# Performance work log

Hardware: AMD Instinct MI355X
Metric: run time of the kernel (lower is better)

## Reference

```python
import jax, jax.numpy as jnp
import numpy as np

B, T, D, H, DK, DV, C, M = 8, 512, 1024, 8, 128, 128, 512, 512
TAU = float(DK) ** 0.5

def _ln(x, g, b, eps=1e-6):
    mu = x.mean(-1, keepdims=True)
    var = ((x - mu) ** 2).mean(-1, keepdims=True)
    return (x - mu) * jax.lax.rsqrt(var + eps) * g + b

def _hln(x, eps=1e-6):
    mu = x.mean(-1, keepdims=True)
    var = ((x - mu) ** 2).mean(-1, keepdims=True)
    return (x - mu) * jax.lax.rsqrt(var + eps)

def setup_inputs() -> dict:
    key = jax.random.key(0)
    ks = jax.random.split(key, 14)
    s = lambda k, shape, fan: jax.random.normal(k, shape, jnp.float32) * (fan ** -0.5)
    return {
        "x": jax.random.normal(ks[0], (B, T, D), jnp.float32),
        "doc_ids": jax.random.randint(ks[1], (B, T), 0, 4),
        "loss_mask": jnp.ones((B, T), jnp.float32),
        "xl_k_hat": jax.random.normal(ks[2], (B, H, M, DK), jnp.float32),
        "xl_v": jax.random.normal(ks[3], (B, H, M, DV), jnp.float32),
        "agg_upper": jax.random.normal(ks[4], (B, H, C, DV), jnp.float32),
        "agg_lower": jax.random.uniform(ks[5], (B, H, C), jnp.float32) * 8.0,
        "w_ln_g": jnp.ones((D,), jnp.float32),
        "w_ln_b": jnp.zeros((D,), jnp.float32),
        "w_q": s(ks[6], (D, H * DK), D),
        "w_k": s(ks[7], (D, H * DK), D),
        "w_v": s(ks[8], (D, H * DV), D),
        "w_g": s(ks[9], (D, H * DV), D),
        "w_res": s(ks[10], (H * DV, D), H * DV),
        "x_u": jax.random.normal(ks[11], (H, DK), jnp.float32) * 0.02,
        "codebook": jax.random.normal(ks[12], (H, C, DK), jnp.float32),
    }

def reference(x, doc_ids, loss_mask, xl_k_hat, xl_v, agg_upper, agg_lower,
              w_ln_g, w_ln_b, w_q, w_k, w_v, w_g, w_res, x_u, codebook):
    # ---- compute_k_q_v_g ----
    xt = _ln(x, w_ln_g, w_ln_b)                                  # [B,T,D]
    q = _hln((xt @ w_q).reshape(B, T, H, DK).transpose(0, 2, 1, 3))  # [B,H,T,DK]
    k = _hln((xt @ w_k).reshape(B, T, H, DK).transpose(0, 2, 1, 3))  # [B,H,T,DK]
    v = (xt @ w_v).reshape(B, T, H, DV).transpose(0, 2, 1, 3)        # [B,H,T,DV]
    g = jax.nn.silu(xt @ w_g)                                        # [B,T,H*DV]

    # ---- vector quantize keys (LearnableVQ) ----
    # dist[b,h,t,c] = ||k - codebook||^2 ; argmin -> shortcodes z
    kc = jnp.einsum('bhtd,hcd->bhtc', k, codebook)
    dist = (k ** 2).sum(-1)[..., None] - 2.0 * kc + (codebook ** 2).sum(-1)[None, :, None, :]
    z = jnp.argmin(dist, axis=-1)                                 # [B,H,T] shortcodes
    k_hat = codebook[jnp.arange(H)[None, :, None], z]             # [B,H,T,DK]
    k_hat_st = k + jax.lax.stop_gradient(k_hat - k)               # straight-through
    mask = loss_mask[:, None, :]                                  # [B,1,T]
    denom_m = mask.sum() * H + 1e-6
    l_commit = (((k - jax.lax.stop_gradient(k_hat)) ** 2).sum(-1) * mask).sum() / denom_m
    l_codebook = (((jax.lax.stop_gradient(k) - k_hat) ** 2).sum(-1) * mask).sum() / denom_m

    # ---- attention over xlcache ++ present, plus aggregated codeword cache ----
    recent_k = jnp.concatenate([xl_k_hat, k_hat_st], axis=2)      # [B,H,M+T,DK]
    recent_v = jnp.concatenate([xl_v, v], axis=2)                 # [B,H,M+T,DV]
    qb = q + x_u[None, :, None, :]
    s_rec = jnp.einsum('bhtd,bhsd->bhts', qb, recent_k) / TAU     # [B,H,T,M+T]
    s_agg = jnp.einsum('bhtd,hcd->bhtc', qb, codebook) / TAU      # [B,H,T,C]

    i = jnp.arange(T)[:, None]
    j = jnp.arange(M + T)[None, :]
    allow = ((j - M) <= i).astype(s_rec.dtype)                    # causal over recent window
    NEG = jnp.asarray(-1e30, s_rec.dtype)
    s_rec_m = jnp.where(allow > 0, s_rec, NEG)

    m = jnp.maximum(s_rec_m.max(-1), s_agg.max(-1))               # [B,H,T]
    a_rec = jnp.exp(s_rec_m - m[..., None]) * allow               # [B,H,T,M+T]
    a_agg = jnp.exp(s_agg - m[..., None])                         # [B,H,T,C]
    den = a_rec.sum(-1) + jnp.einsum('bhtc,bhc->bht', a_agg, agg_lower)
    num = (jnp.einsum('bhts,bhsd->bhtd', a_rec, recent_v)
           + jnp.einsum('bhtc,bhcd->bhtd', a_agg, agg_upper))
    wv = num / den[..., None]                                     # [B,H,T,DV]

    o = wv.transpose(0, 2, 1, 3).reshape(B, T, H * DV) * g        # gated
    res = o @ w_res                                               # [B,T,D]
    return res, l_commit, l_codebook
```

## Files before the change

kernel.cpp:

```cpp
#include <hip/hip_runtime.h>
#include <math.h>

namespace {

constexpr int nB = 8, nT = 512, nD = 1024, nH = 8, nDK = 128, nDV = 128, nC = 512, nM = 512;
constexpr int NROW = nB * nT;
constexpr float RTAU = 0.08838834764831845f;

typedef __attribute__((ext_vector_type(8))) short short8;
typedef __attribute__((ext_vector_type(4))) float f32x4;

__device__ __forceinline__ ushort f2bf(float f) {
  union { float f; uint u; } x; x.f = f;
  uint r = x.u + 0x7fff + ((x.u >> 16) & 1);
  return (ushort)(r >> 16);
}
__device__ __forceinline__ uint pk2(float a, float b) {
  return (uint)f2bf(a) | ((uint)f2bf(b) << 16);
}
__device__ __forceinline__ float bf2f(ushort u) {
  return __uint_as_float(((uint)u) << 16);
}
__device__ __forceinline__ void gload16(const void* g, void* l) {
  __builtin_amdgcn_global_load_lds((const __attribute__((address_space(1))) void*)g,
                                   (__attribute__((address_space(3))) void*)l, 16, 0, 0);
}

constexpr int PREP_LN = 4096;
constexpr int PREP_CAST = PREP_LN + 12288;
constexpr int PREP_WT = PREP_CAST + 1280;
constexpr int PREP_CB = PREP_WT + 2048;

__global__ __launch_bounds__(256) void prep_kernel(
    const float* __restrict__ x, const float* __restrict__ gw, const float* __restrict__ bw,
    ushort* __restrict__ xt_bf,
    const float* __restrict__ xlk, ushort* __restrict__ xlk_bf,
    const float* __restrict__ xlv, ushort* __restrict__ xlv_bf,
    const float* __restrict__ aggU, ushort* __restrict__ aggU_bf,
    const float* __restrict__ wq, const float* __restrict__ wk, const float* __restrict__ wv,
    const float* __restrict__ wg, const float* __restrict__ wres,
    ushort* __restrict__ wqkvg_t, ushort* __restrict__ wres_t,
    const float* __restrict__ cb, float* __restrict__ cbn, ushort* __restrict__ cb_bf) {
  __shared__ float tile[64][65];
  __shared__ float smc[4];
  const int bid = blockIdx.x;
  const int tid = threadIdx.x;

  if (bid < PREP_LN) {
    size_t row = bid;
    float4 v = ((const float4*)(x + row * nD))[tid];
    {
      int lane = tid & 63, w = tid >> 6;
      float s = v.x + v.y + v.z + v.w;
#pragma unroll
      for (int off = 32; off; off >>= 1) s += __shfl_down(s, off);
      if (lane == 0) smc[w] = s;
    }
    __syncthreads();
    float mu = (smc[0] + smc[1] + smc[2] + smc[3]) * (1.f / nD);
    __syncthreads();
    float4 d = make_float4(v.x - mu, v.y - mu, v.z - mu, v.w - mu);
    {
      int lane = tid & 63, w = tid >> 6;
      float s = d.x * d.x + d.y * d.y + d.z * d.z + d.w * d.w;
#pragma unroll
      for (int off = 32; off; off >>= 1) s += __shfl_down(s, off);
      if (lane == 0) smc[w] = s;
    }
    __syncthreads();
    float var = (smc[0] + smc[1] + smc[2] + smc[3]) * (1.f / nD);
    float rs = rsqrtf(var + 1e-6f);
    float4 gg = ((const float4*)gw)[tid];
    float4 bb = ((const float4*)bw)[tid];
    uint2 pb;
    pb.x = pk2(d.x * rs * gg.x + bb.x, d.y * rs * gg.y + bb.y);
    pb.y = pk2(d.z * rs * gg.z + bb.z, d.w * rs * gg.w + bb.w);
    ((uint2*)(xt_bf + row * nD))[tid] = pb;
  } else if (bid < PREP_CAST) {
    const int i = bid - PREP_LN;
    const int which = i >> 12, blk = i & 4095;
    const float* src = which == 0 ? xlk : (which == 1 ? xlv : aggU);
    ushort* dst = which == 0 ? xlk_bf : (which == 1 ? xlv_bf : aggU_bf);
    size_t idx = (size_t)blk * 256 + tid;
    float4 v = ((const float4*)src)[idx];
    uint2 p;
    p.x = pk2(v.x, v.y);
    p.y = pk2(v.z, v.w);
    ((uint2*)dst)[idx] = p;
  } else if (bid < PREP_WT) {
    const int i = bid - PREP_CAST;
    const int z = i >> 8, rem = i & 255;
    const int kz = (rem >> 4) * 64, nz = (rem & 15) * 64;
    const float* W;
    ushort* D;
    if (z == 0)      { W = wq;   D = wqkvg_t; }
    else if (z == 1) { W = wk;   D = wqkvg_t + (size_t)1024 * 1024; }
    else if (z == 2) { W = wv;   D = wqkvg_t + (size_t)2048 * 1024; }
    else if (z == 3) { W = wg;   D = wqkvg_t + (size_t)3072 * 1024; }
    else             { W = wres; D = wres_t; }
    const int c = tid & 63, r4 = tid >> 6;
#pragma unroll
    for (int k = 0; k < 16; ++k) {
      int r = k * 4 + r4;
      tile[r][c] = W[(size_t)(kz + r) * 1024 + nz + c];
    }
    __syncthreads();
#pragma unroll
    for (int k = 0; k < 16; ++k) {
      int n = k * 4 + r4;
      D[(size_t)(nz + n) * 1024 + kz + c] = f2bf(tile[c][n]);
    }
  } else {
    const int i = bid - PREP_WT;
    const int grp = tid >> 7, t128 = tid & 127;
    const int hc = i * 2 + grp;
    float v = cb[(size_t)hc * 128 + t128];
    cb_bf[(size_t)hc * 128 + t128] = f2bf(v);
    float s = v * v;
#pragma unroll
    for (int off = 32; off; off >>= 1) s += __shfl_down(s, off);
    if ((t128 & 63) == 0) smc[grp * 2 + (t128 >> 6)] = s;
    __syncthreads();
    if (t128 == 0) cbn[hc] = smc[grp * 2] + smc[grp * 2 + 1];
  }
}

template <int MODE>
__global__ __launch_bounds__(256) void gemm_bf16_kernel(const ushort* __restrict__ A,
                                                        const ushort* __restrict__ Bt,
                                                        float* __restrict__ C0,
                                                        ushort* __restrict__ C1,
                                                        ushort* __restrict__ C2,
                                                        ushort* __restrict__ C3,
                                                        ushort* __restrict__ kbf,
                                                        float* __restrict__ knorm2,
                                                        const float* __restrict__ xu) {
  __shared__ __align__(16) ushort As[128 * 32];
  __shared__ __align__(16) ushort Bs[128 * 32];
  __shared__ float rowsum[128][2];
  __shared__ float rowsum2[128][2];
  const int tid = threadIdx.x;
  const int w = tid >> 6, l = tid & 63;
  const int lr = l & 15, lg = l >> 4;
  const int wr = w >> 1, wc = w & 1;
  const int n0 = blockIdx.x * 128;
  const int m0 = blockIdx.y * 128;
  constexpr int K = 1024;

  f32x4 acc[4][4];
#pragma unroll
  for (int i = 0; i < 4; ++i)
#pragma unroll
    for (int j = 0; j < 4; ++j) acc[i][j] = (f32x4){0.f, 0.f, 0.f, 0.f};

  const int e0 = w * 512 + l * 8;
  const int r0 = e0 >> 5, c0 = e0 & 31;
  const int e1 = 2048 + e0;
  const int r1 = e1 >> 5, c1 = e1 & 31;
  const ushort* a0p = A + (size_t)(m0 + r0) * K + c0;
  const ushort* a1p = A + (size_t)(m0 + r1) * K + c1;
  const ushort* b0p = Bt + (size_t)(n0 + r0) * K + c0;
  const ushort* b1p = Bt + (size_t)(n0 + r1) * K + c1;
  ushort* lA0 = &As[w * 512];
  ushort* lA1 = &As[2048 + w * 512];
  ushort* lB0 = &Bs[w * 512];
  ushort* lB1 = &Bs[2048 + w * 512];

  for (int k0 = 0; k0 < K; k0 += 32) {
    __syncthreads();
    gload16(a0p + k0, lA0);
    gload16(a1p + k0, lA1);
    gload16(b0p + k0, lB0);
    gload16(b1p + k0, lB1);
    __syncthreads();
    short8 af[4], bfr[4];
#pragma unroll
    for (int i = 0; i < 4; ++i) af[i] = *(const short8*)&As[(wr * 64 + i * 16 + lr) * 32 + lg * 8];
#pragma unroll
    for (int j = 0; j < 4; ++j) bfr[j] = *(const short8*)&Bs[(wc * 64 + j * 16 + lr) * 32 + lg * 8];
    __builtin_amdgcn_s_setprio(1);
#pragma unroll
    for (int i = 0; i < 4; ++i)
#pragma unroll
      for (int j = 0; j < 4; ++j)
        acc[i][j] = __builtin_amdgcn_mfma_f32_16x16x32_bf16(af[i], bfr[j], acc[i][j], 0, 0, 0);
    __builtin_amdgcn_s_setprio(0);
  }

  const int seg = n0 >> 10;
  const int nbase = n0 & 1023;
  if (MODE == 1 && seg <= 1) {
    const int h = nbase >> 7;
    float ps[4][4], ps2[4][4];
#pragma unroll
    for (int i = 0; i < 4; ++i)
#pragma unroll
      for (int r2 = 0; r2 < 4; ++r2) {
        float s = 0.f, s2 = 0.f;
#pragma unroll
        for (int j = 0; j < 4; ++j) {
          float v = acc[i][j][r2];
          s += v;
          s2 += v * v;
        }
#pragma unroll
        for (int off = 1; off < 16; off <<= 1) {
          s += __shfl_xor(s, off);
          s2 += __shfl_xor(s2, off);
        }
        ps[i][r2] = s;
        ps2[i][r2] = s2;
      }
    if (lr == 0) {
#pragma unroll
      for (int i = 0; i < 4; ++i)
#pragma unroll
        for (int r2 = 0; r2 < 4; ++r2) {
          int rloc = wr * 64 + i * 16 + lg * 4 + r2;
          rowsum[rloc][wc] = ps[i][r2];
          rowsum2[rloc][wc] = ps2[i][r2];
        }
    }
    __syncthreads();
#pragma unroll
    for (int i = 0; i < 4; ++i)
#pragma unroll
      for (int r2 = 0; r2 < 4; ++r2) {
        const int rloc = wr * 64 + i * 16 + lg * 4 + r2;
        const int grow = m0 + rloc;
        float tot = rowsum[rloc][0] + rowsum[rloc][1];
        float tot2 = rowsum2[rloc][0] + rowsum2[rloc][1];
        float mu = tot * (1.f / 128.f);
        float qf = tot2 - 128.f * mu * mu;
        float rs = rsqrtf(qf * (1.f / 128.f) + 1e-6f);
#pragma unroll
        for (int j = 0; j < 4; ++j) {
          const int col = wc * 64 + j * 16 + lr;
          float v = (acc[i][j][r2] - mu) * rs;
          if (seg == 0) {
            v += xu[h * 128 + col];
            C1[(size_t)grow * 1024 + nbase + col] = f2bf(v);
          } else {
            kbf[(size_t)grow * 1024 + nbase + col] = f2bf(v);
          }
        }
        if (seg == 1 && lr == 0 && wc == 0) knorm2[(size_t)grow * 8 + h] = qf * rs * rs;
      }
  } else {
#pragma unroll
    for (int i = 0; i < 4; ++i)
#pragma unroll
      for (int j = 0; j < 4; ++j)
#pragma unroll
        for (int r2 = 0; r2 < 4; ++r2) {
          const int row = m0 + wr * 64 + i * 16 + lg * 4 + r2;
          const int col = wc * 64 + j * 16 + lr;
          float v = acc[i][j][r2];
          if (MODE == 0) {
            C0[(size_t)row * 1024 + n0 + col] = v;
          } else {
            const int nloc = nbase + col;
            if (seg == 2) {
              C2[(size_t)row * 1024 + nloc] = f2bf(v);
            } else {
              float s = v / (1.f + __expf(-v));
              C3[(size_t)row * 1024 + nloc] = f2bf(s);
            }
          }
        }
  }
}

__global__ __launch_bounds__(256) void vq_mfma_kernel(const ushort* __restrict__ kbf,
                                                      const ushort* __restrict__ cb_bf,
                                                      const float* __restrict__ cbn,
                                                      const float* __restrict__ knorm2,
                                                      const float* __restrict__ mask,
                                                      ushort* __restrict__ khat_bf,
                                                      float* __restrict__ blocksq) {
  __shared__ ushort Kb[64][136];
  __shared__ ushort Cb[64][136];
  __shared__ float cnsh[64];
  __shared__ int zsh[64];
  __shared__ float dsh[64];
  const int tid = threadIdx.x;
  const int w = tid >> 6, l = tid & 63;
  const int lr = l & 15, lg = l >> 4;
  const int b = blockIdx.y >> 3, h = blockIdx.y & 7;
  const int t0 = blockIdx.x * 64;
  const int srow = tid >> 2, sd = (tid & 3) * 32;

  {
    const ushort* src = kbf + ((size_t)((b * nT + t0 + srow) * nH + h)) * 128 + sd;
    *(uint4*)&Kb[srow][sd] = *(const uint4*)src;
    *(uint4*)&Kb[srow][sd + 8] = *(const uint4*)(src + 8);
    *(uint4*)&Kb[srow][sd + 16] = *(const uint4*)(src + 16);
    *(uint4*)&Kb[srow][sd + 24] = *(const uint4*)(src + 24);
  }
  __syncthreads();

  short8 af[4];
#pragma unroll
  for (int k0 = 0; k0 < 4; ++k0) af[k0] = *(const short8*)&Kb[w * 16 + lr][k0 * 32 + lg * 8];

  float best[4] = {1e30f, 1e30f, 1e30f, 1e30f};
  int bidx[4] = {0, 0, 0, 0};

  for (int cc = 0; cc < 8; ++cc) {
    __syncthreads();
    {
      const ushort* src = cb_bf + ((size_t)(h * nC + cc * 64 + srow)) * 128 + sd;
      *(uint4*)&Cb[srow][sd] = *(const uint4*)src;
      *(uint4*)&Cb[srow][sd + 8] = *(const uint4*)(src + 8);
      *(uint4*)&Cb[srow][sd + 16] = *(const uint4*)(src + 16);
      *(uint4*)&Cb[srow][sd + 24] = *(const uint4*)(src + 24);
      if (tid < 64) cnsh[tid] = cbn[h * nC + cc * 64 + tid];
    }
    __syncthreads();
#pragma unroll
    for (int ct = 0; ct < 4; ++ct) {
      f32x4 z = (f32x4){0.f, 0.f, 0.f, 0.f};
#pragma unroll
      for (int k0 = 0; k0 < 4; ++k0) {
        short8 cf = *(const short8*)&Cb[ct * 16 + lr][k0 * 32 + lg * 8];
        z = __builtin_amdgcn_mfma_f32_16x16x32_bf16(af[k0], cf, z, 0, 0, 0);
      }
      const int code = cc * 64 + ct * 16 + lr;
      const float cn = cnsh[ct * 16 + lr];
#pragma unroll
      for (int r2 = 0; r2 < 4; ++r2) {
        float d = cn - 2.f * z[r2];
        if (d < best[r2]) { best[r2] = d; bidx[r2] = code; }
      }
    }
  }

#pragma unroll
  for (int off = 1; off < 16; off <<= 1) {
#pragma unroll
    for (int r2 = 0; r2 < 4; ++r2) {
      float od = __shfl_xor(best[r2], off);
      int oi = __shfl_xor(bidx[r2], off);
      if (od < best[r2] || (od == best[r2] && oi < bidx[r2])) { best[r2] = od; bidx[r2] = oi; }
    }
  }
  if (lr == 0) {
#pragma unroll
    for (int r2 = 0; r2 < 4; ++r2) {
      int row = w * 16 + lg * 4 + r2;
      zsh[row] = bidx[r2];
      dsh[row] = best[r2];
    }
  }
  __syncthreads();

  {
    const int row = tid >> 2, part = (tid & 3) * 32;
    const ushort* src = cb_bf + ((size_t)(h * nC + zsh[row])) * 128 + part;
    ushort* dst = khat_bf + ((size_t)((b * nT + t0 + row) * nH + h)) * 128 + part;
    *(uint4*)dst = *(const uint4*)src;
    *(uint4*)(dst + 8) = *(const uint4*)(src + 8);
    *(uint4*)(dst + 16) = *(const uint4*)(src + 16);
    *(uint4*)(dst + 24) = *(const uint4*)(src + 24);
  }

  if (tid < 64) {
    float s = mask[b * nT + t0 + tid] *
              (knorm2[(size_t)(b * nT + t0 + tid) * nH + h] + dsh[tid]);
#pragma unroll
    for (int off = 32; off; off >>= 1) s += __shfl_down(s, off);
    if (tid == 0) blocksq[blockIdx.y * gridDim.x + blockIdx.x] = s;
  }
}

__global__ __launch_bounds__(256) void attn_mfma_kernel(
    const ushort* __restrict__ qb, const ushort* __restrict__ khat,
    const ushort* __restrict__ vbuf, const ushort* __restrict__ xlk,
    const ushort* __restrict__ xlv, const ushort* __restrict__ cbb,
    const ushort* __restrict__ aggU, const float* __restrict__ aggL,
    const ushort* __restrict__ gbuf, ushort* __restrict__ o) {
  __shared__ ushort Ks[64][136];
  __shared__ ushort Vts[128][72];
  __shared__ ushort Ps[4][16][72];
  __shared__ float lowb[64];

  const int tid = threadIdx.x;
  const int w = tid >> 6, l = tid & 63;
  const int lr = l & 15, lg = l >> 4;
  const int b = blockIdx.x >> 3, h = blockIdx.x & 7;
  const int t0 = blockIdx.y * 64;

  short8 qf[4];
  {
    const ushort* qrow = qb + ((size_t)((b * nT + t0 + w * 16 + lr) * nH + h)) * 128;
#pragma unroll
    for (int k0 = 0; k0 < 4; ++k0) qf[k0] = *(const short8*)(qrow + k0 * 32 + lg * 8);
  }

  float m_r[4] = {-1e30f, -1e30f, -1e30f, -1e30f};
  float l_r[4] = {0.f, 0.f, 0.f, 0.f};
  f32x4 acc_o[8];
#pragma unroll
  for (int dt = 0; dt < 8; ++dt) acc_o[dt] = (f32x4){0.f, 0.f, 0.f, 0.f};

  const int srow = tid >> 2, sd = (tid & 3) * 32;
  const int kp = tid & 31, dbase = (tid >> 5) * 16;

  auto stageK = [&](const ushort* src) {
#pragma unroll
    for (int q4 = 0; q4 < 4; ++q4)
      *(uint4*)&Ks[srow][sd + q4 * 8] = *(const uint4*)(src + q4 * 8);
  };
  auto stageVbf = [&](const ushort* v0, const ushort* v1) {
    short8 a0 = *(const short8*)(v0);
    short8 a1 = *(const short8*)(v0 + 8);
    short8 b0 = *(const short8*)(v1);
    short8 b1 = *(const short8*)(v1 + 8);
#pragma unroll
    for (int i2 = 0; i2 < 8; ++i2) {
      *(uint*)&Vts[dbase + i2][2 * kp] = (uint)(ushort)a0[i2] | ((uint)(ushort)b0[i2] << 16);
      *(uint*)&Vts[dbase + 8 + i2][2 * kp] = (uint)(ushort)a1[i2] | ((uint)(ushort)b1[i2] << 16);
    }
  };

  auto chunk_body = [&](int sbase, bool AGG, bool MASKQ) {
    f32x4 sc[4];
    __builtin_amdgcn_s_setprio(1);
#pragma unroll
    for (int kt = 0; kt < 4; ++kt) {
      f32x4 z = (f32x4){0.f, 0.f, 0.f, 0.f};
#pragma unroll
      for (int k0 = 0; k0 < 4; ++k0) {
        short8 kf = *(const short8*)&Ks[kt * 16 + lr][k0 * 32 + lg * 8];
        z = __builtin_amdgcn_mfma_f32_16x16x32_bf16(qf[k0], kf, z, 0, 0, 0);
      }
      sc[kt] = z;
    }
    __builtin_amdgcn_s_setprio(0);
    float sv[4][4];
    float pm[4] = {-1e30f, -1e30f, -1e30f, -1e30f};
#pragma unroll
    for (int kt = 0; kt < 4; ++kt)
#pragma unroll
      for (int r2 = 0; r2 < 4; ++r2) {
        float s = sc[kt][r2] * RTAU;
        if (MASKQ) {
          int key = sbase + kt * 16 + lr;
          int tl = t0 + w * 16 + lg * 4 + r2 + nM;
          if (key > tl) s = -1e30f;
        }
        sv[kt][r2] = s;
        pm[r2] = fmaxf(pm[r2], s);
      }
#pragma unroll
    for (int r2 = 0; r2 < 4; ++r2)
#pragma unroll
      for (int off = 1; off < 16; off <<= 1) pm[r2] = fmaxf(pm[r2], __shfl_xor(pm[r2], off));
    float scale[4], rs[4];
#pragma unroll
    for (int r2 = 0; r2 < 4; ++r2) {
      float mn = fmaxf(m_r[r2], pm[r2]);
      scale[r2] = __expf(m_r[r2] - mn);
      m_r[r2] = mn;
      rs[r2] = 0.f;
    }
#pragma unroll
    for (int kt = 0; kt < 4; ++kt)
#pragma unroll
      for (int r2 = 0; r2 < 4; ++r2) {
        float p = __expf(sv[kt][r2] - m_r[r2]);
        rs[r2] += AGG ? p * lowb[kt * 16 + lr] : p;
        Ps[w][lg * 4 + r2][kt * 16 + lr] = f2bf(p);
      }
#pragma unroll
    for (int r2 = 0; r2 < 4; ++r2)
#pragma unroll
      for (int off = 1; off < 16; off <<= 1) rs[r2] += __shfl_xor(rs[r2], off);
#pragma unroll
    for (int r2 = 0; r2 < 4; ++r2) l_r[r2] = l_r[r2] * scale[r2] + rs[r2];
#pragma unroll
    for (int dt = 0; dt < 8; ++dt)
#pragma unroll
      for (int r2 = 0; r2 < 4; ++r2) acc_o[dt][r2] *= scale[r2];
    short8 pa0 = *(const short8*)&Ps[w][lr][lg * 8];
    short8 pa1 = *(const short8*)&Ps[w][lr][32 + lg * 8];
    __builtin_amdgcn_s_setprio(1);
#pragma unroll
    for (int dt = 0; dt < 8; ++dt) {
      short8 vf0 = *(const short8*)&Vts[dt * 16 + lr][lg * 8];
      short8 vf1 = *(const short8*)&Vts[dt * 16 + lr][32 + lg * 8];
      acc_o[dt] = __builtin_amdgcn_mfma_f32_16x16x32_bf16(pa0, vf0, acc_o[dt], 0, 0, 0);
      acc_o[dt] = __builtin_amdgcn_mfma_f32_16x16x32_bf16(pa1, vf1, acc_o[dt], 0, 0, 0);
    }
    __builtin_amdgcn_s_setprio(0);
  };

  const int nch = t0 / 64 + 9;
  for (int ci = 0; ci < nch; ++ci) {
    const int sbase = ci * 64;
    __syncthreads();
    {
      int s = sbase + srow;
      const ushort* src = (s < nM)
          ? xlk + ((size_t)(b * nH + h) * nM + s) * 128 + sd
          : khat + ((size_t)((b * nT + (s - nM)) * nH + h)) * 128 + sd;
      stageK(src);
    }
    {
      int s0 = sbase + 2 * kp;
      if (s0 < nM) {
        const ushort* v0 = xlv + ((size_t)(b * nH + h) * nM + s0) * 128 + dbase;
        stageVbf(v0, v0 + 128);
      } else {
        const ushort* v0 = vbuf + ((size_t)((b * nT + (s0 - nM)) * nH + h)) * 128 + dbase;
        stageVbf(v0, v0 + nH * 128);
      }
    }
    __syncthreads();
    chunk_body(sbase, false, ci == nch - 1);
  }

  for (int ca = 0; ca < 8; ++ca) {
    const int sbase = ca * 64;
    __syncthreads();
    stageK(cbb + ((size_t)h * nC + sbase + srow) * 128 + sd);
    {
      const ushort* v0 = aggU + ((size_t)(b * nH + h) * nC + sbase + 2 * kp) * 128 + dbase;
      stageVbf(v0, v0 + 128);
    }
    if (tid < 64) lowb[tid] = aggL[(size_t)(b * nH + h) * nC + sbase + tid];
    __syncthreads();
    chunk_body(sbase, true, false);
  }

  float inv[4];
#pragma unroll
  for (int r2 = 0; r2 < 4; ++r2) inv[r2] = 1.f / l_r[r2];
#pragma unroll
  for (int dt = 0; dt < 8; ++dt)
#pragma unroll
    for (int r2 = 0; r2 < 4; ++r2) {
      int trow = t0 + w * 16 + lg * 4 + r2;
      size_t oi = ((size_t)(b * nT + trow)) * nD + h * 128 + dt * 16 + lr;
      float gv = bf2f(gbuf[oi]);
      o[oi] = f2bf(acc_o[dt][r2] * inv[r2] * gv);
    }
}

__global__ __launch_bounds__(256) void finalize_kernel(const float* __restrict__ blocksq,
                                                       int nblk,
                                                       const float* __restrict__ mask,
                                                       float* __restrict__ outp) {
  __shared__ float sm[8];
  const int tid = threadIdx.x;
  float s = 0.f, ms = 0.f;
  for (int i = tid; i < NROW; i += 256) {
    if (i < nblk) s += blocksq[i];
    ms += mask[i];
  }
#pragma unroll
  for (int off = 32; off; off >>= 1) { s += __shfl_down(s, off); ms += __shfl_down(ms, off); }
  if ((tid & 63) == 0) { sm[tid >> 6] = s; sm[4 + (tid >> 6)] = ms; }
  __syncthreads();
  if (tid == 0) {
    float ts = sm[0] + sm[1] + sm[2] + sm[3];
    float tm = sm[4] + sm[5] + sm[6] + sm[7];
    float l = ts / (tm * (float)nH + 1e-6f);
    outp[0] = l;
    outp[1] = l;
  }
}

}

extern "C" void kernel_launch(void* const* d_in, const int* in_sizes, int n_in,
                              void* d_out, int out_size, void* d_ws, size_t ws_size,
                              hipStream_t stream) {
  const float* x    = (const float*)d_in[0];
  const float* mask = (const float*)d_in[2];
  const float* xlk  = (const float*)d_in[3];
  const float* xlv  = (const float*)d_in[4];
  const float* aggU = (const float*)d_in[5];
  const float* aggL = (const float*)d_in[6];
  const float* wlng = (const float*)d_in[7];
  const float* wlnb = (const float*)d_in[8];
  const float* wq   = (const float*)d_in[9];
  const float* wk   = (const float*)d_in[10];
  const float* wv   = (const float*)d_in[11];
  const float* wg   = (const float*)d_in[12];
  const float* wres = (const float*)d_in[13];
  const float* xu   = (const float*)d_in[14];
  const float* cb   = (const float*)d_in[15];
  float* out = (float*)d_out;

  float* ws = (float*)d_ws;
  const size_t SZ = (size_t)NROW * nD;
  float*  kregion = ws;
  ushort* qbuf_bf = (ushort*)(ws + SZ);
  ushort* khat_bf = (ushort*)(ws + SZ + SZ / 2);
  ushort* vbuf_bf = (ushort*)(ws + 2 * SZ);
  ushort* gbuf_bf = (ushort*)(ws + 2 * SZ + SZ / 2);
  ushort* xt_bf   = (ushort*)(ws + 3 * SZ);
  ushort* wqkvg_t = (ushort*)(ws + 3 * SZ + SZ / 2);
  ushort* wres_t  = (ushort*)(ws + 4 * SZ);
  ushort* xlk_bf  = (ushort*)(ws + 4 * SZ + SZ / 8);
  ushort* xlv_bf  = (ushort*)(ws + 4 * SZ + SZ / 8 + SZ / 2);
  ushort* aggU_bf = (ushort*)(ws + 4 * SZ + SZ / 8 + SZ);
  ushort* cb_bf   = (ushort*)(ws + 4 * SZ + SZ / 8 + 3 * SZ / 2);
  float*  cbn     = ws + 4 * SZ + SZ / 8 + 3 * SZ / 2 + SZ / 16;
  float*  knorm2  = cbn + 4096;
  float*  bsq     = knorm2 + 32768;
  ushort* kbf     = (ushort*)kregion;
  ushort* obuf_bf = xt_bf;

  prep_kernel<<<PREP_CB, 256, 0, stream>>>(
      x, wlng, wlnb, xt_bf, xlk, xlk_bf, xlv, xlv_bf, aggU, aggU_bf,
      wq, wk, wv, wg, wres, wqkvg_t, wres_t, cb, cbn, cb_bf);

  gemm_bf16_kernel<1><<<dim3(32, 32), 256, 0, stream>>>(
      xt_bf, wqkvg_t, nullptr, qbuf_bf, vbuf_bf, gbuf_bf, kbf, knorm2, xu);

  vq_mfma_kernel<<<dim3(nT / 64, nB * nH), 256, 0, stream>>>(kbf, cb_bf, cbn, knorm2,
                                                             mask, khat_bf, bsq);

  attn_mfma_kernel<<<dim3(nB * nH, nT / 64), 256, 0, stream>>>(
      qbuf_bf, khat_bf, vbuf_bf, xlk_bf, xlv_bf, cb_bf, aggU_bf, aggL, gbuf_bf, obuf_bf);

  gemm_bf16_kernel<0><<<dim3(8, 32), 256, 0, stream>>>(
      obuf_bf, wres_t, out, nullptr, nullptr, nullptr, nullptr, nullptr, nullptr);
  finalize_kernel<<<1, 256, 0, stream>>>(bsq, nT / 64 * nB * nH, mask, out + SZ);
}
```

Measured before the change: 231.2 us.

## Pre-transpose V operands and double-buffer attention staging with async LDS loads

V-like operands (xl_v, agg_upper, and the projected V) are now stored transposed in bf16: the prep kernel does it for xl_v and agg_upper, and the QKV GEMM epilogue does it for V through an LDS tile. The attention kernel then stages K and V^T tiles with direct global-to-LDS loads into XOR-swizzled, double-buffered shared memory, prefetching the next chunk while computing the current one, and uses one barrier per chunk. This removes the per-chunk register-level V transpose and the two-barrier stage-then-compute serialization. In exchange it adds a transposing epilogue with extra syncs in the GEMM, more shared memory (possibly lowering occupancy), and swizzle indexing that must match between writer and reader.

```diff
diff --git a/kernel.cpp b/kernel.cpp
--- a/kernel.cpp
+++ b/kernel.cpp
@@ -25,18 +25,24 @@
   __builtin_amdgcn_global_load_lds((const __attribute__((address_space(1))) void*)g,
                                    (__attribute__((address_space(3))) void*)l, 16, 0, 0);
 }
+__device__ __forceinline__ void gload4(const void* g, void* l) {
+  __builtin_amdgcn_global_load_lds((const __attribute__((address_space(1))) void*)g,
+                                   (__attribute__((address_space(3))) void*)l, 4, 0, 0);
+}
 
 constexpr int PREP_LN = 4096;
-constexpr int PREP_CAST = PREP_LN + 12288;
-constexpr int PREP_WT = PREP_CAST + 1280;
-constexpr int PREP_CB = PREP_WT + 2048;
+constexpr int PREP_XLK = PREP_LN + 4096;
+constexpr int PREP_XLVT = PREP_XLK + 1024;
+constexpr int PREP_AGGUT = PREP_XLVT + 1024;
+constexpr int PREP_WT = PREP_AGGUT + 1280;
+constexpr int PREP_TOTAL = PREP_WT + 2048;
 
 __global__ __launch_bounds__(256) void prep_kernel(
     const float* __restrict__ x, const float* __restrict__ gw, const float* __restrict__ bw,
     ushort* __restrict__ xt_bf,
     const float* __restrict__ xlk, ushort* __restrict__ xlk_bf,
-    const float* __restrict__ xlv, ushort* __restrict__ xlv_bf,
-    const float* __restrict__ aggU, ushort* __restrict__ aggU_bf,
+    const float* __restrict__ xlv, ushort* __restrict__ xlvT,
+    const float* __restrict__ aggU, ushort* __restrict__ aggUT,
     const float* __restrict__ wq, const float* __restrict__ wk, const float* __restrict__ wv,
     const float* __restrict__ wg, const float* __restrict__ wres,
     ushort* __restrict__ wqkvg_t, ushort* __restrict__ wres_t,
@@ -76,19 +82,37 @@
     pb.x = pk2(d.x * rs * gg.x + bb.x, d.y * rs * gg.y + bb.y);
     pb.y = pk2(d.z * rs * gg.z + bb.z, d.w * rs * gg.w + bb.w);
     ((uint2*)(xt_bf + row * nD))[tid] = pb;
-  } else if (bid < PREP_CAST) {
-    const int i = bid - PREP_LN;
-    const int which = i >> 12, blk = i & 4095;
-    const float* src = which == 0 ? xlk : (which == 1 ? xlv : aggU);
-    ushort* dst = which == 0 ? xlk_bf : (which == 1 ? xlv_bf : aggU_bf);
+  } else if (bid < PREP_XLK) {
+    const int blk = bid - PREP_LN;
     size_t idx = (size_t)blk * 256 + tid;
-    float4 v = ((const float4*)src)[idx];
+    float4 v = ((const float4*)xlk)[idx];
     uint2 p;
     p.x = pk2(v.x, v.y);
     p.y = pk2(v.z, v.w);
-    ((uint2*)dst)[idx] = p;
+    ((uint2*)xlk_bf)[idx] = p;
+  } else if (bid < PREP_AGGUT) {
+    const bool isXlv = bid < PREP_XLVT;
+    const int i = bid - (isXlv ? PREP_XLK : PREP_XLVT);
+    const float* S = isXlv ? xlv : aggU;
+    ushort* D = isXlv ? xlvT : aggUT;
+    const int bh = i >> 4, t = i & 15;
+    const int tok0 = (t >> 1) * 64, d0 = (t & 1) * 64;
+    const float* src = S + ((size_t)bh * 512 + tok0) * 128 + d0;
+    ushort* dst = D + ((size_t)bh * 128 + d0) * 512 + tok0;
+    const int c = tid & 63, r4 = tid >> 6;
+#pragma unroll
+    for (int k = 0; k < 16; ++k) {
+      int r = k * 4 + r4;
+      tile[r][c] = src[(size_t)r * 128 + c];
+    }
+    __syncthreads();
+#pragma unroll
+    for (int k = 0; k < 16; ++k) {
+      int dd = k * 4 + r4;
+      dst[(size_t)dd * 512 + c] = f2bf(tile[c][dd]);
+    }
   } else if (bid < PREP_WT) {
-    const int i = bid - PREP_CAST;
+    const int i = bid - PREP_AGGUT;
     const int z = i >> 8, rem = i & 255;
     const int kz = (rem >> 4) * 64, nz = (rem & 15) * 64;
     const float* W;
@@ -139,6 +163,7 @@
   __shared__ __align__(16) ushort Bs[128 * 32];
   __shared__ float rowsum[128][2];
   __shared__ float rowsum2[128][2];
+  __shared__ __align__(16) ushort tbuf[128][72];
   const int tid = threadIdx.x;
   const int w = tid >> 6, l = tid & 63;
   const int lr = l & 15, lg = l >> 4;
@@ -246,6 +271,37 @@
         }
         if (seg == 1 && lr == 0 && wc == 0) knorm2[(size_t)grow * 8 + h] = qf * rs * rs;
       }
+  } else if (MODE == 1 && seg == 2) {
+    const int h = nbase >> 7;
+    const int bq = m0 >> 9;
+    const int tokbase = m0 & 511;
+#pragma unroll
+    for (int half = 0; half < 2; ++half) {
+      __syncthreads();
+      if (wr == half) {
+#pragma unroll
+        for (int i = 0; i < 4; ++i)
+#pragma unroll
+          for (int j = 0; j < 4; ++j)
+#pragma unroll
+            for (int r2 = 0; r2 < 4; ++r2) {
+              const int col = wc * 64 + j * 16 + lr;
+              const int rl = i * 16 + lg * 4 + r2;
+              tbuf[col][rl] = f2bf(acc[i][j][r2]);
+            }
+      }
+      __syncthreads();
+      {
+        const int d = tid >> 1;
+        const int hrow = tid & 1;
+        ushort* gdst = C2 + (((size_t)(bq * 8 + h) * 128 + d) * 512
+                             + tokbase + half * 64 + hrow * 32);
+        const ushort* lsrc = &tbuf[d][hrow * 32];
+#pragma unroll
+        for (int q = 0; q < 4; ++q)
+          *(uint4*)(gdst + q * 8) = *(const uint4*)(lsrc + q * 8);
+      }
+    }
   } else {
 #pragma unroll
     for (int i = 0; i < 4; ++i)
@@ -259,13 +315,8 @@
           if (MODE == 0) {
             C0[(size_t)row * 1024 + n0 + col] = v;
           } else {
-            const int nloc = nbase + col;
-            if (seg == 2) {
-              C2[(size_t)row * 1024 + nloc] = f2bf(v);
-            } else {
-              float s = v / (1.f + __expf(-v));
-              C3[(size_t)row * 1024 + nloc] = f2bf(s);
-            }
+            float s = v / (1.f + __expf(-v));
+            C3[(size_t)row * 1024 + nbase + col] = f2bf(s);
           }
         }
   }
@@ -375,14 +426,14 @@
 
 __global__ __launch_bounds__(256) void attn_mfma_kernel(
     const ushort* __restrict__ qb, const ushort* __restrict__ khat,
-    const ushort* __restrict__ vbuf, const ushort* __restrict__ xlk,
-    const ushort* __restrict__ xlv, const ushort* __restrict__ cbb,
-    const ushort* __restrict__ aggU, const float* __restrict__ aggL,
+    const ushort* __restrict__ vbufT, const ushort* __restrict__ xlk,
+    const ushort* __restrict__ xlvT, const ushort* __restrict__ cbb,
+    const ushort* __restrict__ aggUT, const float* __restrict__ aggL,
     const ushort* __restrict__ gbuf, ushort* __restrict__ o) {
-  __shared__ ushort Ks[64][136];
-  __shared__ ushort Vts[128][72];
+  __shared__ __align__(16) ushort Ks[2][64][128];
+  __shared__ __align__(16) ushort Vts[2][128][64];
   __shared__ ushort Ps[4][16][72];
-  __shared__ float lowb[64];
+  __shared__ float lowb[2][64];
 
   const int tid = threadIdx.x;
   const int w = tid >> 6, l = tid & 63;
@@ -403,35 +454,65 @@
 #pragma unroll
   for (int dt = 0; dt < 8; ++dt) acc_o[dt] = (f32x4){0.f, 0.f, 0.f, 0.f};
 
-  const int srow = tid >> 2, sd = (tid & 3) * 32;
-  const int kp = tid & 31, dbase = (tid >> 5) * 16;
-
-  auto stageK = [&](const ushort* src) {
-#pragma unroll
-    for (int q4 = 0; q4 < 4; ++q4)
-      *(uint4*)&Ks[srow][sd + q4 * 8] = *(const uint4*)(src + q4 * 8);
+  const int nch = t0 / 64 + 9;
+  const int ntot = nch + 8;
+
+  auto stage = [&](int ci) {
+    const int buf = ci & 1;
+    const bool isAgg = ci >= nch;
+    const int sb = isAgg ? (ci - nch) * 64 : ci * 64;
+    char* kdst = (char*)&Ks[buf][0][0];
+    char* vdst = (char*)&Vts[buf][0][0];
+#pragma unroll
+    for (int j = 0; j < 4; ++j) {
+      {
+        const int row = w * 16 + j * 4 + (l >> 4);
+        const int scol = ((l & 15) * 16) ^ ((row & 7) << 4);
+        const ushort* srow;
+        if (isAgg) {
+          srow = cbb + ((size_t)(h * nC + sb + row)) * 128;
+        } else {
+          const int s = sb + row;
+          srow = (s < nM) ? xlk + ((size_t)(b * nH + h) * nM + s) * 128
+                          : khat + ((size_t)((b * nT + (s - nM)) * nH + h)) * 128;
+        }
+        gload16((const char*)srow + scol, kdst + w * 4096 + j * 1024);
+      }
+      {
+        const int d = w * 32 + j * 8 + (l >> 3);
+        const int skb = ((l & 7) * 16) ^ ((d & 7) << 4);
+        const ushort* srow;
+        if (isAgg) {
+          srow = aggUT + (((size_t)(b * nH + h) * 128 + d) * 512 + sb);
+        } else if (sb < nM) {
+          srow = xlvT + (((size_t)(b * nH + h) * 128 + d) * 512 + sb);
+        } else {
+          srow = vbufT + (((size_t)(b * nH + h) * 128 + d) * 512 + (sb - nM));
+        }
+        gload16((const char*)srow + skb, vdst + w * 4096 + j * 1024);
+      }
+    }
+    if (isAgg && w == 0) {
+      gload4(aggL + (size_t)(b * nH + h) * nC + sb + l, &lowb[buf][0]);
+    }
   };
-  auto stageVbf = [&](const ushort* v0, const ushort* v1) {
-    short8 a0 = *(const short8*)(v0);
-    short8 a1 = *(const short8*)(v0 + 8);
-    short8 b0 = *(const short8*)(v1);
-    short8 b1 = *(const short8*)(v1 + 8);
-#pragma unroll
-    for (int i2 = 0; i2 < 8; ++i2) {
-      *(uint*)&Vts[dbase + i2][2 * kp] = (uint)(ushort)a0[i2] | ((uint)(ushort)b0[i2] << 16);
-      *(uint*)&Vts[dbase + 8 + i2][2 * kp] = (uint)(ushort)a1[i2] | ((uint)(ushort)b1[i2] << 16);
-    }
-  };
-
-  auto chunk_body = [&](int sbase, bool AGG, bool MASKQ) {
+
+  auto chunk_body = [&](int ci) {
+    const int buf = ci & 1;
+    const bool AGG = ci >= nch;
+    const bool MASKQ = ci == nch - 1;
+    const int sbase = AGG ? 0 : ci * 64;
+    const char* ksb = (const char*)&Ks[buf][0][0];
+    const char* vsb = (const char*)&Vts[buf][0][0];
     f32x4 sc[4];
     __builtin_amdgcn_s_setprio(1);
 #pragma unroll
     for (int kt = 0; kt < 4; ++kt) {
       f32x4 z = (f32x4){0.f, 0.f, 0.f, 0.f};
+      const int R = kt * 16 + lr;
 #pragma unroll
       for (int k0 = 0; k0 < 4; ++k0) {
-        short8 kf = *(const short8*)&Ks[kt * 16 + lr][k0 * 32 + lg * 8];
+        short8 kf = *(const short8*)(ksb + R * 256 + ((k0 * 64 + lg * 16) ^ ((R & 7) << 4)));
         z = __builtin_amdgcn_mfma_f32_16x16x32_bf16(qf[k0], kf, z, 0, 0, 0);
       }
       sc[kt] = z;
@@ -469,7 +550,7 @@
 #pragma unroll
       for (int r2 = 0; r2 < 4; ++r2) {
         float p = __expf(sv[kt][r2] - m_r[r2]);
-        rs[r2] += AGG ? p * lowb[kt * 16 + lr] : p;
+        rs[r2] += AGG ? p * lowb[buf][kt * 16 + lr] : p;
         Ps[w][lg * 4 + r2][kt * 16 + lr] = f2bf(p);
       }
 #pragma unroll
@@ -487,50 +568,21 @@
     __builtin_amdgcn_s_setprio(1);
 #pragma unroll
     for (int dt = 0; dt < 8; ++dt) {
-      short8 vf0 = *(const short8*)&Vts[dt * 16 + lr][lg * 8];
-      short8 vf1 = *(const short8*)&Vts[dt * 16 + lr][32 + lg * 8];
+      const int R2 = dt * 16 + lr;
+      short8 vf0 = *(const short8*)(vsb + R2 * 128 + ((lg * 16) ^ ((R2 & 7) << 4)));
+      short8 vf1 = *(const short8*)(vsb + R2 * 128 + ((64 + lg * 16) ^ ((R2 & 7) << 4)));
       acc_o[dt] = __builtin_amdgcn_mfma_f32_16x16x32_bf16(pa0, vf0, acc_o[dt], 0, 0, 0);
       acc_o[dt] = __builtin_amdgcn_mfma_f32_16x16x32_bf16(pa1, vf1, acc_o[dt], 0, 0, 0);
     }
     __builtin_amdgcn_s_setprio(0);
   };
 
-  const int nch = t0 / 64 + 9;
-  for (int ci = 0; ci < nch; ++ci) {
-    const int sbase = ci * 64;
-    __syncthreads();
-    {
-      int s = sbase + srow;
-      const ushort* src = (s < nM)
-          ? xlk + ((size_t)(b * nH + h) * nM + s) * 128 + sd
-          : khat + ((size_t)((b * nT + (s - nM)) * nH + h)) * 128 + sd;
-      stageK(src);
-    }
-    {
-      int s0 = sbase + 2 * kp;
-      if (s0 < nM) {
-        const ushort* v0 = xlv + ((size_t)(b * nH + h) * nM + s0) * 128 + dbase;
-        stageVbf(v0, v0 + 128);
-      } else {
-        const ushort* v0 = vbuf + ((size_t)((b * nT + (s0 - nM)) * nH + h)) * 128 + dbase;
-        stageVbf(v0, v0 + nH * 128);
-      }
-    }
-    __syncthreads();
-    chunk_body(sbase, false, ci == nch - 1);
-  }
-
-  for (int ca = 0; ca < 8; ++ca) {
-    const int sbase = ca * 64;
-    __syncthreads();
-    stageK(cbb + ((size_t)h * nC + sbase + srow) * 128 + sd);
-    {
-      const ushort* v0 = aggU + ((size_t)(b * nH + h) * nC + sbase + 2 * kp) * 128 + dbase;
-      stageVbf(v0, v0 + 128);
-    }
-    if (tid < 64) lowb[tid] = aggL[(size_t)(b * nH + h) * nC + sbase + tid];
-    __syncthreads();
-    chunk_body(sbase, true, false);
+  stage(0);
+  __syncthreads();
+  for (int ci = 0; ci < ntot; ++ci) {
+    if (ci + 1 < ntot) stage(ci + 1);
+    chunk_body(ci);
+    __syncthreads();
   }
 
   float inv[4];
@@ -598,14 +650,14 @@
   float*  kregion = ws;
   ushort* qbuf_bf = (ushort*)(ws + SZ);
   ushort* khat_bf = (ushort*)(ws + SZ + SZ / 2);
-  ushort* vbuf_bf = (ushort*)(ws + 2 * SZ);
+  ushort* vbufT   = (ushort*)(ws + 2 * SZ);
   ushort* gbuf_bf = (ushort*)(ws + 2 * SZ + SZ / 2);
   ushort* xt_bf   = (ushort*)(ws + 3 * SZ);
   ushort* wqkvg_t = (ushort*)(ws + 3 * SZ + SZ / 2);
   ushort* wres_t  = (ushort*)(ws + 4 * SZ);
   ushort* xlk_bf  = (ushort*)(ws + 4 * SZ + SZ / 8);
-  ushort* xlv_bf  = (ushort*)(ws + 4 * SZ + SZ / 8 + SZ / 2);
-  ushort* aggU_bf = (ushort*)(ws + 4 * SZ + SZ / 8 + SZ);
+  ushort* xlvT    = (ushort*)(ws + 4 * SZ + SZ / 8 + SZ / 2);
+  ushort* aggUT   = (ushort*)(ws + 4 * SZ + SZ / 8 + SZ);
   ushort* cb_bf   = (ushort*)(ws + 4 * SZ + SZ / 8 + 3 * SZ / 2);
   float*  cbn     = ws + 4 * SZ + SZ / 8 + 3 * SZ / 2 + SZ / 16;
   float*  knorm2  = cbn + 4096;
@@ -613,18 +665,18 @@
   ushort* kbf     = (ushort*)kregion;
   ushort* obuf_bf = xt_bf;
 
-  prep_kernel<<<PREP_CB, 256, 0, stream>>>(
-      x, wlng, wlnb, xt_bf, xlk, xlk_bf, xlv, xlv_bf, aggU, aggU_bf,
+  prep_kernel<<<PREP_TOTAL, 256, 0, stream>>>(
+      x, wlng, wlnb, xt_bf, xlk, xlk_bf, xlv, xlvT, aggU, aggUT,
       wq, wk, wv, wg, wres, wqkvg_t, wres_t, cb, cbn, cb_bf);
 
   gemm_bf16_kernel<1><<<dim3(32, 32), 256, 0, stream>>>(
-      xt_bf, wqkvg_t, nullptr, qbuf_bf, vbuf_bf, gbuf_bf, kbf, knorm2, xu);
+      xt_bf, wqkvg_t, nullptr, qbuf_bf, vbufT, gbuf_bf, kbf, knorm2, xu);
 
   vq_mfma_kernel<<<dim3(nT / 64, nB * nH), 256, 0, stream>>>(kbf, cb_bf, cbn, knorm2,
                                                              mask, khat_bf, bsq);
 
   attn_mfma_kernel<<<dim3(nB * nH, nT / 64), 256, 0, stream>>>(
-      qbuf_bf, khat_bf, vbuf_bf, xlk_bf, xlv_bf, cb_bf, aggU_bf, aggL, gbuf_bf, obuf_bf);
+      qbuf_bf, khat_bf, vbufT, xlk_bf, xlvT, cb_bf, aggUT, aggL, gbuf_bf, obuf_bf);
 
   gemm_bf16_kernel<0><<<dim3(8, 32), 256, 0, stream>>>(
       obuf_bf, wres_t, out, nullptr, nullptr, nullptr, nullptr, nullptr, nullptr);
```

Measured after the change: 275.5 us. 19.1% more time.

## Double GEMM K-tile to 64 and XOR-swizzle LDS layout

Applied to the files above, without the earlier changes.

The bf16 projection GEMM now stages 64-wide K slices per iteration instead of 32, which halves the number of barrier pairs per K loop. The LDS tiles get an XOR swizzle on the 16-byte column chunk by row, applied on the global source offset during the direct-to-LDS load and undone on the read, to avoid bank conflicts on the fragment loads. LDS usage per block doubles, which may lower occupancy, and there is still no double buffering.

```diff
diff --git a/kernel.cpp b/kernel.cpp
--- a/kernel.cpp
+++ b/kernel.cpp
@@ -135,8 +135,8 @@
                                                         ushort* __restrict__ kbf,
                                                         float* __restrict__ knorm2,
                                                         const float* __restrict__ xu) {
-  __shared__ __align__(16) ushort As[128 * 32];
-  __shared__ __align__(16) ushort Bs[128 * 32];
+  __shared__ __align__(16) ushort As[128 * 64];
+  __shared__ __align__(16) ushort Bs[128 * 64];
   __shared__ float rowsum[128][2];
   __shared__ float rowsum2[128][2];
   const int tid = threadIdx.x;
@@ -153,38 +153,47 @@
 #pragma unroll
     for (int j = 0; j < 4; ++j) acc[i][j] = (f32x4){0.f, 0.f, 0.f, 0.f};
 
-  const int e0 = w * 512 + l * 8;
-  const int r0 = e0 >> 5, c0 = e0 & 31;
-  const int e1 = 2048 + e0;
-  const int r1 = e1 >> 5, c1 = e1 & 31;
-  const ushort* a0p = A + (size_t)(m0 + r0) * K + c0;
-  const ushort* a1p = A + (size_t)(m0 + r1) * K + c1;
-  const ushort* b0p = Bt + (size_t)(n0 + r0) * K + c0;
-  const ushort* b1p = Bt + (size_t)(n0 + r1) * K + c1;
-  ushort* lA0 = &As[w * 512];
-  ushort* lA1 = &As[2048 + w * 512];
-  ushort* lB0 = &Bs[w * 512];
-  ushort* lB1 = &Bs[2048 + w * 512];
-
-  for (int k0 = 0; k0 < K; k0 += 32) {
-    __syncthreads();
-    gload16(a0p + k0, lA0);
-    gload16(a1p + k0, lA1);
-    gload16(b0p + k0, lB0);
-    gload16(b1p + k0, lB1);
-    __syncthreads();
-    short8 af[4], bfr[4];
-#pragma unroll
-    for (int i = 0; i < 4; ++i) af[i] = *(const short8*)&As[(wr * 64 + i * 16 + lr) * 32 + lg * 8];
-#pragma unroll
-    for (int j = 0; j < 4; ++j) bfr[j] = *(const short8*)&Bs[(wc * 64 + j * 16 + lr) * 32 + lg * 8];
-    __builtin_amdgcn_s_setprio(1);
-#pragma unroll
-    for (int i = 0; i < 4; ++i)
-#pragma unroll
-      for (int j = 0; j < 4; ++j)
-        acc[i][j] = __builtin_amdgcn_mfma_f32_16x16x32_bf16(af[i], bfr[j], acc[i][j], 0, 0, 0);
-    __builtin_amdgcn_s_setprio(0);
+  const int eb = w * 512 + l * 8;
+  int rowA[4], sof[4], eo[4];
+#pragma unroll
+  for (int r = 0; r < 4; ++r) {
+    int e = r * 2048 + eb;
+    rowA[r] = e >> 6;
+    eo[r] = e * 2;
+    sof[r] = ((e & 63) * 2) ^ ((rowA[r] & 7) << 4);
+  }
+
+  for (int k0 = 0; k0 < K; k0 += 64) {
+    __syncthreads();
+#pragma unroll
+    for (int r = 0; r < 4; ++r) {
+      gload16((const char*)(A + (size_t)(m0 + rowA[r]) * K + k0) + sof[r], (char*)As + eo[r]);
+      gload16((const char*)(Bt + (size_t)(n0 + rowA[r]) * K + k0) + sof[r], (char*)Bs + eo[r]);
+    }
+    __syncthreads();
+#pragma unroll
+    for (int kk = 0; kk < 2; ++kk) {
+      short8 af[4], bfr[4];
+#pragma unroll
+      for (int i = 0; i < 4; ++i) {
+        const int row = wr * 64 + i * 16 + lr;
+        af[i] = *(const short8*)((const char*)As + row * 128 +
+                                 ((kk * 64 + lg * 16) ^ ((row & 7) << 4)));
+      }
+#pragma unroll
+      for (int j = 0; j < 4; ++j) {
+        const int row = wc * 64 + j * 16 + lr;
+        bfr[j] = *(const short8*)((const char*)Bs + row * 128 +
+                                  ((kk * 64 + lg * 16) ^ ((row & 7) << 4)));
+      }
+      __builtin_amdgcn_s_setprio(1);
+#pragma unroll
+      for (int i = 0; i < 4; ++i)
+#pragma unroll
+        for (int j = 0; j < 4; ++j)
+          acc[i][j] = __builtin_amdgcn_mfma_f32_16x16x32_bf16(af[i], bfr[j], acc[i][j], 0, 0, 0);
+      __builtin_amdgcn_s_setprio(0);
+    }
   }
 
   const int seg = n0 >> 10;
```

Result: faster. 219.4 us (-5.1%).
